# Kernel optimization log

Hardware: AMD Instinct MI355X
Metric: run time of the kernel (lower is better)

Reference implementation:

```python
import jax, jax.numpy as jnp
import numpy as np

M, N, EMB, H, ENC, T = 4096, 256, 64, 128, 128, 100


def _lstm_dir(x, Wih, Whh, b, h0, c0):
    # x: (T, M, E); PyTorch LSTM gate order i, f, g, o
    def step(carry, xt):
        h, c = carry
        g = xt @ Wih + h @ Whh + b
        i, f, gg, o = jnp.split(g, 4, axis=-1)
        c = jax.nn.sigmoid(f) * c + jax.nn.sigmoid(i) * jnp.tanh(gg)
        h = jax.nn.sigmoid(o) * jnp.tanh(c)
        return (h, c), h
    _, hs = jax.lax.scan(step, (h0, c0), x)
    return hs  # (T, M, H)


def setup_inputs() -> dict:
    key = jax.random.key(0)
    ks = jax.random.split(key, 14)
    rn = lambda k, sh, s: jax.random.normal(k, sh, jnp.float32) * s
    return {
        "lane_features": jax.random.normal(ks[0], (M, 600), jnp.float32),
        "obs_encoding": jax.random.normal(ks[1], (N, 128), jnp.float32),
        "embed_W": rn(ks[2], (4, EMB), 0.5),
        "embed_b": jnp.zeros((EMB,), jnp.float32),
        "attn_W": rn(ks[3], (128, 100), 0.09),
        "attn_b": jnp.zeros((100,), jnp.float32),
        "Wih_f": rn(ks[4], (EMB, 4 * H), 0.08),
        "Whh_f": rn(ks[5], (H, 4 * H), 0.08),
        "b_f": jnp.zeros((4 * H,), jnp.float32),
        "Wih_b": rn(ks[6], (EMB, 4 * H), 0.08),
        "Whh_b": rn(ks[7], (H, 4 * H), 0.08),
        "b_b": jnp.zeros((4 * H,), jnp.float32),
        "h0": rn(ks[8], (2, 1, H), 0.1),
        "c0": rn(ks[9], (2, 1, H), 0.1),
        "enc_W": rn(ks[10], (8 * H, ENC), 0.03),
        "enc_b": jnp.zeros((ENC,), jnp.float32),
        "same_obs_mask": jax.random.randint(ks[11], (M, 1), 0, N, jnp.int32),
    }


def reference(lane_features, obs_encoding, embed_W, embed_b, attn_W, attn_b,
              Wih_f, Whh_f, b_f, Wih_b, Whh_b, b_b, h0, c0, enc_W, enc_b,
              same_obs_mask):
    Mloc = lane_features.shape[0]
    E = embed_W.shape[1]
    Hh = Whh_f.shape[0]
    # last 400 features -> 100 timesteps x 4 features, then embed + relu
    feat = lane_features[:, -400:].reshape(Mloc * 100, 4)
    lane_embed = jax.nn.relu(feat @ embed_W + embed_b).reshape(Mloc, 100, E)
    # per-obstacle attention over the 100 lane points
    scores = jax.nn.softmax(jax.nn.relu(obs_encoding @ attn_W + attn_b), axis=1)  # (N, 100)
    # the original per-obs_id scatter loop == a single gather by obstacle id
    att = scores[same_obs_mask[:, 0]]  # (M, 100)
    x = jnp.transpose(lane_embed, (1, 0, 2))  # (T, M, E)
    h0f = jnp.broadcast_to(h0[0], (Mloc, Hh)); c0f = jnp.broadcast_to(c0[0], (Mloc, Hh))
    h0b = jnp.broadcast_to(h0[1], (Mloc, Hh)); c0b = jnp.broadcast_to(c0[1], (Mloc, Hh))
    hs_f = _lstm_dir(x, Wih_f, Whh_f, b_f, h0f, c0f)
    hs_b = _lstm_dir(x[::-1], Wih_b, Whh_b, b_b, h0b, c0b)[::-1]
    ls = jnp.transpose(jnp.concatenate([hs_f, hs_b], axis=-1), (1, 0, 2))  # (M, T, 2H)
    front = ls[:, 0, :]
    back = ls[:, -1, :]
    mx = jnp.max(ls, axis=1)
    attn_states = jnp.sum(ls * att[:, :, None], axis=1)
    out = jnp.concatenate([front, back, mx, attn_states], axis=1)  # (M, 8H)
    return jax.nn.relu(out @ enc_W + enc_b)
```

## Files before the change

kernel.cpp:

```cpp
#include <hip/hip_runtime.h>
#include <hip/hip_bf16.h>

#define MROWS 4096
#define TSTEPS 100
#define EMB 64
#define HID 128
#define GATES 512
#define KTOT 192
#define ROWS_PB 32
#define SROW 200
#define PSTR 520

typedef _Float16 half8 __attribute__((ext_vector_type(8)));
typedef _Float16 half4v __attribute__((ext_vector_type(4)));
typedef float f32x4 __attribute__((ext_vector_type(4)));

#define LOG2E  1.44269504f
#define LOG2E2 2.88539008f

__device__ __forceinline__ float rcpf(float x) { return __builtin_amdgcn_rcpf(x); }
__device__ __forceinline__ float ex2(float x) { return __builtin_amdgcn_exp2f(x); }

__global__ void prep_kernel(const float* __restrict__ obs,
                            const float* __restrict__ attn_W,
                            const float* __restrict__ attn_b,
                            float* __restrict__ scores,
                            const float* __restrict__ enc_W,
                            _Float16* __restrict__ frag) {
    const int tid = threadIdx.x;
    if (blockIdx.x < 256) {
        const int row = blockIdx.x;
        __shared__ float obs_s[128];
        __shared__ float red[128];

        if (tid < 128) obs_s[tid] = obs[row * 128 + tid];
        __syncthreads();

        float s = -1e30f;
        if (tid < 100) {
            float a = attn_b[tid];
            #pragma unroll 4
            for (int k = 0; k < 128; k++) a += obs_s[k] * attn_W[k * 100 + tid];
            s = fmaxf(a, 0.f);
        }
        if (tid < 128) red[tid] = s;
        __syncthreads();
        for (int off = 64; off > 0; off >>= 1) {
            if (tid < off) red[tid] = fmaxf(red[tid], red[tid + off]);
            __syncthreads();
        }
        const float m = red[0];
        __syncthreads();
        const float e = (tid < 100) ? __expf(s - m) : 0.f;
        if (tid < 128) red[tid] = e;
        __syncthreads();
        for (int off = 64; off > 0; off >>= 1) {
            if (tid < off) red[tid] += red[tid + off];
            __syncthreads();
        }
        const float inv = __fdividef(1.f, red[0]);
        if (tid < 100) scores[row * 100 + tid] = e * inv;
    } else {
        const int pb = blockIdx.x - 256;
        const int pair = pb * 16 + (tid >> 4);
        const int tile = pair >> 5;
        const int it   = pair & 31;
        const int sub  = tid & 15;
        #pragma unroll
        for (int li = 0; li < 4; li++) {
            const int l = sub * 4 + li;
            const int c = tile * 16 + (l & 15);
            const int kbase = it * 32 + (l >> 4) * 8;
            half8 v;
            #pragma unroll
            for (int j = 0; j < 8; j++) v[j] = (_Float16)enc_W[(kbase + j) * 128 + c];
            *(half8*)(frag + (((long)(tile * 32 + it)) * 64 + l) * 8) = v;
        }
    }
}

__launch_bounds__(512, 2)
__global__ void lstm_kernel(const float* __restrict__ lane_features,
                            const float* __restrict__ embed_W,
                            const float* __restrict__ embed_b,
                            const float* __restrict__ Wih_f,
                            const float* __restrict__ Whh_f,
                            const float* __restrict__ b_f,
                            const float* __restrict__ Wih_b,
                            const float* __restrict__ Whh_b,
                            const float* __restrict__ b_b,
                            const float* __restrict__ h0,
                            const float* __restrict__ c0,
                            const int*   __restrict__ mask,
                            const float* __restrict__ scores,
                            const _Float16* __restrict__ frag,
                            float* __restrict__ pacc) {
    const int blk = blockIdx.x;
    const int d = blk >> 7;
    const int rowbase = (blk & 127) * ROWS_PB;
    const int tid = threadIdx.x;
    const int wave = tid >> 6;
    const int lane = tid & 63;
    const int lane16 = lane & 15;
    const int quad = lane >> 4;

    const float* Wih = d ? Wih_b : Wih_f;
    const float* Whh = d ? Whh_b : Whh_f;
    const float* bia = d ? b_b : b_f;

    __shared__ __attribute__((aligned(16))) char smem[38400];
    auto panel = (_Float16 (*)[ROWS_PB][SROW])smem;
    float (*att_s)[32] = (float (*)[32])(smem + 25600);
    _Float16* pool = (_Float16*)smem;

    const int erow = tid >> 4;
    const int cc = (tid & 15) * 4;
    float ew_r[4][4], eb_r[4];
    #pragma unroll
    for (int j = 0; j < 4; j++) {
        #pragma unroll
        for (int jj = 0; jj < 4; jj++) ew_r[j][jj] = embed_W[j * EMB + cc + jj];
    }
    #pragma unroll
    for (int jj = 0; jj < 4; jj++) eb_r[jj] = embed_b[cc + jj];

    {
        const int r = tid >> 4, tcol = tid & 15;
        const int mr = mask[rowbase + r];
        for (int t = tcol; t < 100; t += 16) att_s[t][r] = scores[mr * 100 + t];
    }

    const int unitg = wave * 16 + lane16;
    half8 Bf[24];
    #pragma unroll
    for (int ct = 0; ct < 4; ct++) {
        const float scale = (ct == 2) ? LOG2E2 : LOG2E;
        const int col = ct * 128 + unitg;
        #pragma unroll
        for (int ki = 0; ki < 6; ki++) {
            half8 b;
            #pragma unroll
            for (int j = 0; j < 8; j++) {
                const int kk = ki * 32 + quad * 8 + j;
                const float w = (kk < EMB) ? Wih[kk * GATES + col]
                                           : Whh[(kk - EMB) * GATES + col];
                b[j] = (_Float16)(w * scale);
            }
            Bf[ct * 6 + ki] = b;
        }
    }
    f32x4 biasacc[4];
    #pragma unroll
    for (int ct = 0; ct < 4; ct++) {
        const float bg = bia[ct * 128 + unitg] * ((ct == 2) ? LOG2E2 : LOG2E);
        biasacc[ct] = (f32x4){bg, bg, bg, bg};
    }

    float cst[8], mx[8], as[8], h0s[8], hl[8];
    const float cinit = c0[d * 128 + unitg];
    #pragma unroll
    for (int p = 0; p < 8; p++) {
        cst[p] = cinit; mx[p] = -1e30f; as[p] = 0.f; h0s[p] = 0.f; hl[p] = 0.f;
    }

    for (int idx = tid; idx < ROWS_PB * HID; idx += 512) {
        const int r = idx >> 7, u = idx & 127;
        panel[0][r][EMB + u] = (_Float16)h0[d * 128 + u];
    }

    {
        const int t0 = d ? (TSTEPS - 1) : 0;
        const float4 fv = *(const float4*)(lane_features + (long)(rowbase + erow) * 600 + 200 + 4 * t0);
        half4v hv;
        #pragma unroll
        for (int jj = 0; jj < 4; jj++) {
            float e = eb_r[jj] + fv.x * ew_r[0][jj] + fv.y * ew_r[1][jj]
                               + fv.z * ew_r[2][jj] + fv.w * ew_r[3][jj];
            hv[jj] = (_Float16)fmaxf(e, 0.f);
        }
        *(half4v*)&panel[0][erow][cc] = hv;
    }
    __syncthreads();

    const float* fptr = lane_features + (long)(rowbase + erow) * 600 + 200
                      + (d ? 4 * (TSTEPS - 2) : 4);
    const int fstep = d ? -4 : 4;

#define HALF_STEP(PB, SE)                                                      \
    {                                                                          \
        const int se = (SE);                                                   \
        const int t = d ? (TSTEPS - 1 - se) : se;                              \
        float4 fv;                                                             \
        if (se < TSTEPS - 1) { fv = *(const float4*)fptr; fptr += fstep; }     \
        const f32x4 awv0 = *(const f32x4*)&att_s[t][quad * 4];                 \
        const f32x4 awv1 = *(const f32x4*)&att_s[t][16 + quad * 4];            \
        f32x4 acc[2][4];                                                       \
        _Pragma("unroll")                                                      \
        for (int ki = 0; ki < 6; ki++) {                                       \
            const half8 a0 = *(const half8*)&panel[PB][lane16][ki * 32 + quad * 8];      \
            const half8 a1 = *(const half8*)&panel[PB][16 + lane16][ki * 32 + quad * 8]; \
            _Pragma("unroll")                                                  \
            for (int ct = 0; ct < 4; ct++) {                                   \
                if (ki == 0) {                                                 \
                    acc[0][ct] = __builtin_amdgcn_mfma_f32_16x16x32_f16(a0, Bf[ct * 6], biasacc[ct], 0, 0, 0); \
                    acc[1][ct] = __builtin_amdgcn_mfma_f32_16x16x32_f16(a1, Bf[ct * 6], biasacc[ct], 0, 0, 0); \
                } else {                                                       \
                    acc[0][ct] = __builtin_amdgcn_mfma_f32_16x16x32_f16(a0, Bf[ct * 6 + ki], acc[0][ct], 0, 0, 0); \
                    acc[1][ct] = __builtin_amdgcn_mfma_f32_16x16x32_f16(a1, Bf[ct * 6 + ki], acc[1][ct], 0, 0, 0); \
                }                                                              \
            }                                                                  \
        }                                                                      \
        _Pragma("unroll")                                                      \
        for (int rt = 0; rt < 2; rt++) {                                       \
            _Pragma("unroll")                                                  \
            for (int r = 0; r < 4; r++) {                                      \
                const int pp = rt * 4 + r;                                     \
                const int row_local = rt * 16 + quad * 4 + r;                  \
                const float gi = acc[rt][0][r];                                \
                const float gf = acc[rt][1][r];                                \
                const float gg = fminf(acc[rt][2][r], 80.f);                   \
                const float go = acc[rt][3][r];                                \
                const float Ei = ex2(-gi);                                     \
                const float Ef = ex2(-gf);                                     \
                const float Eg = ex2(gg);                                      \
                const float Eo = ex2(-go);                                     \
                const float sf = rcpf(1.f + Ef);                               \
                const float r1 = rcpf((1.f + Ei) * (Eg + 1.f));                \
                const float cn = sf * cst[pp] + (Eg - 1.f) * r1;               \
                const float Ec = ex2(fminf(cn * LOG2E2, 80.f));                \
                const float r2 = rcpf((1.f + Eo) * (Ec + 1.f));                \
                const float h = (Ec - 1.f) * r2;                               \
                cst[pp] = cn;                                                  \
                hl[pp] = h;                                                    \
                mx[pp] = fmaxf(mx[pp], h);                                     \
                as[pp] = fmaf((rt ? awv1 : awv0)[r], h, as[pp]);               \
                panel[1 - (PB)][row_local][EMB + unitg] = (_Float16)h;         \
            }                                                                  \
        }                                                                      \
        if (se == 0) {                                                         \
            _Pragma("unroll")                                                  \
            for (int pp = 0; pp < 8; pp++) h0s[pp] = hl[pp];                   \
        }                                                                      \
        if (se < TSTEPS - 1) {                                                 \
            half4v hv;                                                         \
            _Pragma("unroll")                                                  \
            for (int jj = 0; jj < 4; jj++) {                                   \
                float e = eb_r[jj] + fv.x * ew_r[0][jj] + fv.y * ew_r[1][jj]   \
                                   + fv.z * ew_r[2][jj] + fv.w * ew_r[3][jj];  \
                hv[jj] = (_Float16)fmaxf(e, 0.f);                              \
            }                                                                  \
            *(half4v*)&panel[1 - (PB)][erow][cc] = hv;                         \
        }                                                                      \
        __syncthreads();                                                       \
    }

    for (int s = 0; s < TSTEPS; s += 2) {
        HALF_STEP(0, s)
        HALF_STEP(1, s + 1)
    }
#undef HALF_STEP

    #pragma unroll
    for (int pp = 0; pp < 8; pp++) {
        const int row_local = (pp >> 2) * 16 + quad * 4 + (pp & 3);
        const float fr = d ? hl[pp] : h0s[pp];
        const float bk = d ? h0s[pp] : hl[pp];
        pool[row_local * PSTR + 0 * 128 + unitg] = (_Float16)fr;
        pool[row_local * PSTR + 1 * 128 + unitg] = (_Float16)bk;
        pool[row_local * PSTR + 2 * 128 + unitg] = (_Float16)mx[pp];
        pool[row_local * PSTR + 3 * 128 + unitg] = (_Float16)as[pp];
    }
    __syncthreads();

    f32x4 cacc0 = {0.f, 0.f, 0.f, 0.f}, cacc1 = {0.f, 0.f, 0.f, 0.f};
    const _Float16* fbase = frag + ((long)wave * 32) * 64 * 8 + lane * 8;
    #pragma unroll
    for (int lc = 0; lc < 16; lc++) {
        const int seg = lc >> 2, c = lc & 3;
        const int itg = seg * 8 + d * 4 + c;
        const half8 b  = *(const half8*)(fbase + (long)itg * 64 * 8);
        const half8 a0 = *(const half8*)&pool[lane16 * PSTR + lc * 32 + quad * 8];
        const half8 a1 = *(const half8*)&pool[(16 + lane16) * PSTR + lc * 32 + quad * 8];
        cacc0 = __builtin_amdgcn_mfma_f32_16x16x32_f16(a0, b, cacc0, 0, 0, 0);
        cacc1 = __builtin_amdgcn_mfma_f32_16x16x32_f16(a1, b, cacc1, 0, 0, 0);
    }
    float* pacc_d = pacc + (long)d * MROWS * 128;
    #pragma unroll
    for (int r = 0; r < 4; r++) {
        pacc_d[(long)(rowbase + quad * 4 + r) * 128 + wave * 16 + lane16]      = cacc0[r];
        pacc_d[(long)(rowbase + 16 + quad * 4 + r) * 128 + wave * 16 + lane16] = cacc1[r];
    }
}

__global__ void final_kernel(const float* __restrict__ pacc,
                             const float* __restrict__ enc_b,
                             float* __restrict__ out) {
    const int idx = (blockIdx.x * 256 + threadIdx.x) * 4;
    const float4 a = *(const float4*)(pacc + idx);
    const float4 b = *(const float4*)(pacc + (long)MROWS * 128 + idx);
    const float4 bb = *(const float4*)(enc_b + (idx & 127));
    float4 o;
    o.x = fmaxf(a.x + b.x + bb.x, 0.f);
    o.y = fmaxf(a.y + b.y + bb.y, 0.f);
    o.z = fmaxf(a.z + b.z + bb.z, 0.f);
    o.w = fmaxf(a.w + b.w + bb.w, 0.f);
    *(float4*)(out + idx) = o;
}

extern "C" void kernel_launch(void* const* d_in, const int* in_sizes, int n_in,
                              void* d_out, int out_size, void* d_ws, size_t ws_size,
                              hipStream_t stream) {
    const float* lane_features = (const float*)d_in[0];
    const float* obs_encoding  = (const float*)d_in[1];
    const float* embed_W = (const float*)d_in[2];
    const float* embed_b = (const float*)d_in[3];
    const float* attn_W  = (const float*)d_in[4];
    const float* attn_b  = (const float*)d_in[5];
    const float* Wih_f   = (const float*)d_in[6];
    const float* Whh_f   = (const float*)d_in[7];
    const float* b_f     = (const float*)d_in[8];
    const float* Wih_b   = (const float*)d_in[9];
    const float* Whh_b   = (const float*)d_in[10];
    const float* b_b     = (const float*)d_in[11];
    const float* h0      = (const float*)d_in[12];
    const float* c0      = (const float*)d_in[13];
    const float* enc_W   = (const float*)d_in[14];
    const float* enc_b   = (const float*)d_in[15];
    const int*   mask    = (const int*)d_in[16];

    float*     scores = (float*)d_ws;
    _Float16*  frag   = (_Float16*)((char*)d_ws + (128 << 10));
    float*     pacc   = (float*)((char*)d_ws + (512 << 10));
    float*     out    = (float*)d_out;

    prep_kernel<<<272, 256, 0, stream>>>(obs_encoding, attn_W, attn_b, scores,
                                         enc_W, frag);
    lstm_kernel<<<256, 512, 0, stream>>>(lane_features, embed_W, embed_b,
                                         Wih_f, Whh_f, b_f, Wih_b, Whh_b, b_b,
                                         h0, c0, mask, scores, frag, pacc);
    final_kernel<<<512, 256, 0, stream>>>(pacc, enc_b, out);
}
```

Before: 286.9 us.

## Fuse attention softmax and final epilogue into LSTM kernel with atomic accumulation

Removes the separate attention-score pass by having each LSTM block compute the softmax attention for its own rows directly from obs_encoding. It also drops the final kernel: the two direction blocks atomically add their partial encoder outputs into a zeroed buffer, and the second block to arrive, detected through a per-tile counter, applies bias and ReLU. The prep kernel now only builds the fp16 fragments, staging them through shared memory, and zeroes pacc and the flags. In exchange, the attention work is recomputed redundantly per row in both directions, and the last-arriver pattern has no memory fence, so it may read stale pacc values.

```diff
diff --git a/kernel.cpp b/kernel.cpp
--- a/kernel.cpp
+++ b/kernel.cpp
@@ -21,61 +21,44 @@
 __device__ __forceinline__ float rcpf(float x) { return __builtin_amdgcn_rcpf(x); }
 __device__ __forceinline__ float ex2(float x) { return __builtin_amdgcn_exp2f(x); }
 
-__global__ void prep_kernel(const float* __restrict__ obs,
-                            const float* __restrict__ attn_W,
-                            const float* __restrict__ attn_b,
-                            float* __restrict__ scores,
-                            const float* __restrict__ enc_W,
-                            _Float16* __restrict__ frag) {
+__global__ void frag_prep_kernel(const float* __restrict__ enc_W,
+                                 _Float16* __restrict__ frag,
+                                 float* __restrict__ pacc,
+                                 int* __restrict__ flags) {
     const int tid = threadIdx.x;
-    if (blockIdx.x < 256) {
-        const int row = blockIdx.x;
-        __shared__ float obs_s[128];
-        __shared__ float red[128];
-
-        if (tid < 128) obs_s[tid] = obs[row * 128 + tid];
-        __syncthreads();
-
-        float s = -1e30f;
-        if (tid < 100) {
-            float a = attn_b[tid];
-            #pragma unroll 4
-            for (int k = 0; k < 128; k++) a += obs_s[k] * attn_W[k * 100 + tid];
-            s = fmaxf(a, 0.f);
-        }
-        if (tid < 128) red[tid] = s;
-        __syncthreads();
-        for (int off = 64; off > 0; off >>= 1) {
-            if (tid < off) red[tid] = fmaxf(red[tid], red[tid + off]);
-            __syncthreads();
-        }
-        const float m = red[0];
-        __syncthreads();
-        const float e = (tid < 100) ? __expf(s - m) : 0.f;
-        if (tid < 128) red[tid] = e;
-        __syncthreads();
-        for (int off = 64; off > 0; off >>= 1) {
-            if (tid < off) red[tid] += red[tid + off];
-            __syncthreads();
-        }
-        const float inv = __fdividef(1.f, red[0]);
-        if (tid < 100) scores[row * 100 + tid] = e * inv;
-    } else {
-        const int pb = blockIdx.x - 256;
-        const int pair = pb * 16 + (tid >> 4);
-        const int tile = pair >> 5;
-        const int it   = pair & 31;
-        const int sub  = tid & 15;
-        #pragma unroll
-        for (int li = 0; li < 4; li++) {
-            const int l = sub * 4 + li;
-            const int c = tile * 16 + (l & 15);
-            const int kbase = it * 32 + (l >> 4) * 8;
-            half8 v;
-            #pragma unroll
-            for (int j = 0; j < 8; j++) v[j] = (_Float16)enc_W[(kbase + j) * 128 + c];
-            *(half8*)(frag + (((long)(tile * 32 + it)) * 64 + l) * 8) = v;
-        }
+    if (blockIdx.x >= 16) {
+        const int z = blockIdx.x - 16;
+        const float4 zero = {0.f, 0.f, 0.f, 0.f};
+        #pragma unroll
+        for (int i = 0; i < 8; i++) {
+            *(float4*)(pacc + (long)z * 8192 + (i * 256 + tid) * 4) = zero;
+        }
+        if (blockIdx.x == 16 && tid < 128) flags[tid] = 0;
+        return;
+    }
+    const int pb = blockIdx.x;
+    __shared__ float tile[64][132];
+    #pragma unroll
+    for (int i = 0; i < 32; i++) {
+        const int idx = i * 256 + tid;
+        const int rr = idx >> 7, ccol = idx & 127;
+        tile[rr][ccol] = enc_W[(pb * 64 + rr) * 128 + ccol];
+    }
+    __syncthreads();
+    const int pair = tid >> 4;
+    const int tl = pair >> 1;
+    const int itl = pair & 1;
+    const int it = pb * 2 + itl;
+    const int sub = tid & 15;
+    #pragma unroll
+    for (int li = 0; li < 4; li++) {
+        const int l = sub * 4 + li;
+        const int c = tl * 16 + (l & 15);
+        const int kb = itl * 32 + (l >> 4) * 8;
+        half8 v;
+        #pragma unroll
+        for (int j = 0; j < 8; j++) v[j] = (_Float16)tile[kb + j][c];
+        *(half8*)(frag + (((long)(tl * 32 + it)) * 64 + l) * 8) = v;
     }
 }
 
@@ -92,9 +75,14 @@
                             const float* __restrict__ h0,
                             const float* __restrict__ c0,
                             const int*   __restrict__ mask,
-                            const float* __restrict__ scores,
+                            const float* __restrict__ obs,
+                            const float* __restrict__ attn_W,
+                            const float* __restrict__ attn_b,
+                            const float* __restrict__ enc_b,
                             const _Float16* __restrict__ frag,
-                            float* __restrict__ pacc) {
+                            float* __restrict__ pacc,
+                            int* __restrict__ flags,
+                            float* __restrict__ out) {
     const int blk = blockIdx.x;
     const int d = blk >> 7;
     const int rowbase = (blk & 127) * ROWS_PB;
@@ -111,6 +99,7 @@
     __shared__ __attribute__((aligned(16))) char smem[38400];
     auto panel = (_Float16 (*)[ROWS_PB][SROW])smem;
     float (*att_s)[32] = (float (*)[32])(smem + 25600);
+    float (*red)[16] = (float (*)[16])(smem + 12800);
     _Float16* pool = (_Float16*)smem;
 
     const int erow = tid >> 4;
@@ -125,9 +114,55 @@
     for (int jj = 0; jj < 4; jj++) eb_r[jj] = embed_b[cc + jj];
 
     {
-        const int r = tid >> 4, tcol = tid & 15;
+        const int r = tid >> 4;
+        const int tcol = tid & 15;
         const int mr = mask[rowbase + r];
-        for (int t = tcol; t < 100; t += 16) att_s[t][r] = scores[mr * 100 + t];
+        const float* obsrow = obs + mr * 128;
+        float a[7];
+        #pragma unroll
+        for (int j = 0; j < 7; j++) {
+            const int t = tcol + j * 16;
+            a[j] = (t < 100) ? attn_b[t] : 0.f;
+        }
+        #pragma unroll 4
+        for (int k = 0; k < 128; k++) {
+            const float ov = obsrow[k];
+            #pragma unroll
+            for (int j = 0; j < 7; j++) {
+                const int t = tcol + j * 16;
+                a[j] = fmaf(ov, attn_W[k * 100 + (t < 100 ? t : 99)], a[j]);
+            }
+        }
+        float s_loc[7];
+        float lm = -1e30f;
+        #pragma unroll
+        for (int j = 0; j < 7; j++) {
+            const int t = tcol + j * 16;
+            s_loc[j] = (t < 100) ? fmaxf(a[j], 0.f) : -1e30f;
+            lm = fmaxf(lm, s_loc[j]);
+        }
+        red[r][tcol] = lm;
+        __syncthreads();
+        float m = -1e30f;
+        #pragma unroll
+        for (int j = 0; j < 16; j++) m = fmaxf(m, red[r][j]);
+        __syncthreads();
+        float ls = 0.f;
+        #pragma unroll
+        for (int j = 0; j < 7; j++) {
+            if (tcol + j * 16 < 100) ls += ex2((s_loc[j] - m) * LOG2E);
+        }
+        red[r][tcol] = ls;
+        __syncthreads();
+        float Z = 0.f;
+        #pragma unroll
+        for (int j = 0; j < 16; j++) Z += red[r][j];
+        const float rz = rcpf(Z);
+        #pragma unroll
+        for (int j = 0; j < 7; j++) {
+            const int t = tcol + j * 16;
+            if (t < 100) att_s[t][r] = ex2((s_loc[j] - m) * LOG2E) * rz;
+        }
     }
 
     const int unitg = wave * 16 + lane16;
@@ -284,27 +319,27 @@
         cacc0 = __builtin_amdgcn_mfma_f32_16x16x32_f16(a0, b, cacc0, 0, 0, 0);
         cacc1 = __builtin_amdgcn_mfma_f32_16x16x32_f16(a1, b, cacc1, 0, 0, 0);
     }
-    float* pacc_d = pacc + (long)d * MROWS * 128;
+
+    const int col = wave * 16 + lane16;
     #pragma unroll
     for (int r = 0; r < 4; r++) {
-        pacc_d[(long)(rowbase + quad * 4 + r) * 128 + wave * 16 + lane16]      = cacc0[r];
-        pacc_d[(long)(rowbase + 16 + quad * 4 + r) * 128 + wave * 16 + lane16] = cacc1[r];
-    }
-}
-
-__global__ void final_kernel(const float* __restrict__ pacc,
-                             const float* __restrict__ enc_b,
-                             float* __restrict__ out) {
-    const int idx = (blockIdx.x * 256 + threadIdx.x) * 4;
-    const float4 a = *(const float4*)(pacc + idx);
-    const float4 b = *(const float4*)(pacc + (long)MROWS * 128 + idx);
-    const float4 bb = *(const float4*)(enc_b + (idx & 127));
-    float4 o;
-    o.x = fmaxf(a.x + b.x + bb.x, 0.f);
-    o.y = fmaxf(a.y + b.y + bb.y, 0.f);
-    o.z = fmaxf(a.z + b.z + bb.z, 0.f);
-    o.w = fmaxf(a.w + b.w + bb.w, 0.f);
-    *(float4*)(out + idx) = o;
+        atomicAdd(&pacc[(long)(rowbase + quad * 4 + r) * 128 + col], cacc0[r]);
+        atomicAdd(&pacc[(long)(rowbase + 16 + quad * 4 + r) * 128 + col], cacc1[r]);
+    }
+    __syncthreads();
+    int* lf = (int*)smem;
+    if (tid == 0) lf[0] = atomicAdd(&flags[blk & 127], 1);
+    __syncthreads();
+    if (lf[0] == 1) {
+        const float bb = enc_b[col];
+        #pragma unroll
+        for (int r = 0; r < 4; r++) {
+            const long i0 = (long)(rowbase + quad * 4 + r) * 128 + col;
+            const long i1 = (long)(rowbase + 16 + quad * 4 + r) * 128 + col;
+            out[i0] = fmaxf(pacc[i0] + bb, 0.f);
+            out[i1] = fmaxf(pacc[i1] + bb, 0.f);
+        }
+    }
 }
 
 extern "C" void kernel_launch(void* const* d_in, const int* in_sizes, int n_in,
@@ -328,15 +363,14 @@
     const float* enc_b   = (const float*)d_in[15];
     const int*   mask    = (const int*)d_in[16];
 
-    float*     scores = (float*)d_ws;
-    _Float16*  frag   = (_Float16*)((char*)d_ws + (128 << 10));
-    float*     pacc   = (float*)((char*)d_ws + (512 << 10));
-    float*     out    = (float*)d_out;
-
-    prep_kernel<<<272, 256, 0, stream>>>(obs_encoding, attn_W, attn_b, scores,
-                                         enc_W, frag);
+    _Float16*  frag  = (_Float16*)d_ws;
+    int*       flags = (int*)((char*)d_ws + (256 << 10));
+    float*     pacc  = (float*)((char*)d_ws + (512 << 10));
+    float*     out   = (float*)d_out;
+
+    frag_prep_kernel<<<80, 256, 0, stream>>>(enc_W, frag, pacc, flags);
     lstm_kernel<<<256, 512, 0, stream>>>(lane_features, embed_W, embed_b,
                                          Wih_f, Whh_f, b_f, Wih_b, Whh_b, b_b,
-                                         h0, c0, mask, scores, frag, pacc);
-    final_kernel<<<512, 256, 0, stream>>>(pacc, enc_b, out);
+                                         h0, c0, mask, obs_encoding, attn_W,
+                                         attn_b, enc_b, frag, pacc, flags, out);
 }
```

After: 291.8 us. No clear change (+1.7%).

## Fuse final reduction into LSTM kernel via atomics and last-block flag

Applied to the files above, without the earlier changes.

Removes the separate final kernel. Each direction block now atomically adds its partial encoder output into a zeroed accumulator, and whichever of the two blocks for a row tile arrives second (found through a counter flag) applies bias and ReLU and writes the output. The prep kernel gains extra blocks that zero the accumulator and flags, and its enc_W transpose now goes through shared memory for coalesced loads. The LSTM cell step is also reordered so the first row tile's MFMAs finish before the second's, letting gate math overlap with the remaining matrix work. The costs are global atomics and a last-arriver pattern whose correctness depends on memory ordering between the atomic adds and the flag increment.

```diff
diff --git a/kernel.cpp b/kernel.cpp
--- a/kernel.cpp
+++ b/kernel.cpp
@@ -26,7 +26,9 @@
                             const float* __restrict__ attn_b,
                             float* __restrict__ scores,
                             const float* __restrict__ enc_W,
-                            _Float16* __restrict__ frag) {
+                            _Float16* __restrict__ frag,
+                            float* __restrict__ pacc,
+                            int* __restrict__ flags) {
     const int tid = threadIdx.x;
     if (blockIdx.x < 256) {
         const int row = blockIdx.x;
@@ -60,22 +62,39 @@
         }
         const float inv = __fdividef(1.f, red[0]);
         if (tid < 100) scores[row * 100 + tid] = e * inv;
-    } else {
+    } else if (blockIdx.x < 272) {
         const int pb = blockIdx.x - 256;
-        const int pair = pb * 16 + (tid >> 4);
-        const int tile = pair >> 5;
-        const int it   = pair & 31;
-        const int sub  = tid & 15;
+        __shared__ float tile[64][132];
+        #pragma unroll
+        for (int i = 0; i < 32; i++) {
+            const int idx = i * 256 + tid;
+            const int rr = idx >> 7, ccol = idx & 127;
+            tile[rr][ccol] = enc_W[(pb * 64 + rr) * 128 + ccol];
+        }
+        __syncthreads();
+        const int pair = tid >> 4;
+        const int tl = pair >> 1;
+        const int itl = pair & 1;
+        const int it = pb * 2 + itl;
+        const int sub = tid & 15;
         #pragma unroll
         for (int li = 0; li < 4; li++) {
             const int l = sub * 4 + li;
-            const int c = tile * 16 + (l & 15);
-            const int kbase = it * 32 + (l >> 4) * 8;
+            const int c = tl * 16 + (l & 15);
+            const int kb = itl * 32 + (l >> 4) * 8;
             half8 v;
             #pragma unroll
-            for (int j = 0; j < 8; j++) v[j] = (_Float16)enc_W[(kbase + j) * 128 + c];
-            *(half8*)(frag + (((long)(tile * 32 + it)) * 64 + l) * 8) = v;
-        }
+            for (int j = 0; j < 8; j++) v[j] = (_Float16)tile[kb + j][c];
+            *(half8*)(frag + (((long)(tl * 32 + it)) * 64 + l) * 8) = v;
+        }
+    } else {
+        const int z = blockIdx.x - 272;
+        const float4 zero = {0.f, 0.f, 0.f, 0.f};
+        #pragma unroll
+        for (int i = 0; i < 8; i++) {
+            *(float4*)(pacc + (long)z * 8192 + (i * 256 + tid) * 4) = zero;
+        }
+        if (blockIdx.x == 272 && tid < 128) flags[tid] = 0;
     }
 }
 
@@ -93,8 +112,11 @@
                             const float* __restrict__ c0,
                             const int*   __restrict__ mask,
                             const float* __restrict__ scores,
+                            const float* __restrict__ enc_b,
                             const _Float16* __restrict__ frag,
-                            float* __restrict__ pacc) {
+                            float* __restrict__ pacc,
+                            int* __restrict__ flags,
+                            float* __restrict__ out) {
     const int blk = blockIdx.x;
     const int d = blk >> 7;
     const int rowbase = (blk & 127) * ROWS_PB;
@@ -186,57 +208,60 @@
                       + (d ? 4 * (TSTEPS - 2) : 4);
     const int fstep = d ? -4 : 4;
 
+#define CELL_RT(RT, ACC, AWV)                                                  \
+    _Pragma("unroll")                                                          \
+    for (int r = 0; r < 4; r++) {                                              \
+        const int pp = (RT) * 4 + r;                                           \
+        const int row_local = (RT) * 16 + quad * 4 + r;                        \
+        const float gi = ACC[0][r];                                            \
+        const float gf = ACC[1][r];                                            \
+        const float gg = fminf(ACC[2][r], 80.f);                               \
+        const float go = ACC[3][r];                                            \
+        const float Ei = ex2(-gi);                                             \
+        const float Ef = ex2(-gf);                                             \
+        const float Eg = ex2(gg);                                              \
+        const float Eo = ex2(-go);                                             \
+        const float sf = rcpf(1.f + Ef);                                       \
+        const float r1 = rcpf((1.f + Ei) * (Eg + 1.f));                        \
+        const float cn = sf * cst[pp] + (Eg - 1.f) * r1;                       \
+        const float Ec = ex2(fminf(cn * LOG2E2, 80.f));                        \
+        const float r2 = rcpf((1.f + Eo) * (Ec + 1.f));                        \
+        const float h = (Ec - 1.f) * r2;                                       \
+        cst[pp] = cn;                                                          \
+        hl[pp] = h;                                                            \
+        mx[pp] = fmaxf(mx[pp], h);                                             \
+        as[pp] = fmaf((AWV)[r], h, as[pp]);                                    \
+        panel[1 - (PB_)][row_local][EMB + unitg] = (_Float16)h;                \
+    }
+
 #define HALF_STEP(PB, SE)                                                      \
     {                                                                          \
+        const int PB_ = (PB);                                                  \
         const int se = (SE);                                                   \
         const int t = d ? (TSTEPS - 1 - se) : se;                              \
         float4 fv;                                                             \
         if (se < TSTEPS - 1) { fv = *(const float4*)fptr; fptr += fstep; }     \
         const f32x4 awv0 = *(const f32x4*)&att_s[t][quad * 4];                 \
         const f32x4 awv1 = *(const f32x4*)&att_s[t][16 + quad * 4];            \
-        f32x4 acc[2][4];                                                       \
+        f32x4 acc0[4], acc1[4];                                                \
         _Pragma("unroll")                                                      \
         for (int ki = 0; ki < 6; ki++) {                                       \
             const half8 a0 = *(const half8*)&panel[PB][lane16][ki * 32 + quad * 8];      \
+            _Pragma("unroll")                                                  \
+            for (int ct = 0; ct < 4; ct++)                                     \
+                acc0[ct] = __builtin_amdgcn_mfma_f32_16x16x32_f16(             \
+                    a0, Bf[ct * 6 + ki], (ki == 0) ? biasacc[ct] : acc0[ct], 0, 0, 0); \
+        }                                                                      \
+        _Pragma("unroll")                                                      \
+        for (int ki = 0; ki < 6; ki++) {                                       \
             const half8 a1 = *(const half8*)&panel[PB][16 + lane16][ki * 32 + quad * 8]; \
             _Pragma("unroll")                                                  \
-            for (int ct = 0; ct < 4; ct++) {                                   \
-                if (ki == 0) {                                                 \
-                    acc[0][ct] = __builtin_amdgcn_mfma_f32_16x16x32_f16(a0, Bf[ct * 6], biasacc[ct], 0, 0, 0); \
-                    acc[1][ct] = __builtin_amdgcn_mfma_f32_16x16x32_f16(a1, Bf[ct * 6], biasacc[ct], 0, 0, 0); \
-                } else {                                                       \
-                    acc[0][ct] = __builtin_amdgcn_mfma_f32_16x16x32_f16(a0, Bf[ct * 6 + ki], acc[0][ct], 0, 0, 0); \
-                    acc[1][ct] = __builtin_amdgcn_mfma_f32_16x16x32_f16(a1, Bf[ct * 6 + ki], acc[1][ct], 0, 0, 0); \
-                }                                                              \
-            }                                                                  \
+            for (int ct = 0; ct < 4; ct++)                                     \
+                acc1[ct] = __builtin_amdgcn_mfma_f32_16x16x32_f16(             \
+                    a1, Bf[ct * 6 + ki], (ki == 0) ? biasacc[ct] : acc1[ct], 0, 0, 0); \
         }                                                                      \
-        _Pragma("unroll")                                                      \
-        for (int rt = 0; rt < 2; rt++) {                                       \
-            _Pragma("unroll")                                                  \
-            for (int r = 0; r < 4; r++) {                                      \
-                const int pp = rt * 4 + r;                                     \
-                const int row_local = rt * 16 + quad * 4 + r;                  \
-                const float gi = acc[rt][0][r];                                \
-                const float gf = acc[rt][1][r];                                \
-                const float gg = fminf(acc[rt][2][r], 80.f);                   \
-                const float go = acc[rt][3][r];                                \
-                const float Ei = ex2(-gi);                                     \
-                const float Ef = ex2(-gf);                                     \
-                const float Eg = ex2(gg);                                      \
-                const float Eo = ex2(-go);                                     \
-                const float sf = rcpf(1.f + Ef);                               \
-                const float r1 = rcpf((1.f + Ei) * (Eg + 1.f));                \
-                const float cn = sf * cst[pp] + (Eg - 1.f) * r1;               \
-                const float Ec = ex2(fminf(cn * LOG2E2, 80.f));                \
-                const float r2 = rcpf((1.f + Eo) * (Ec + 1.f));                \
-                const float h = (Ec - 1.f) * r2;                               \
-                cst[pp] = cn;                                                  \
-                hl[pp] = h;                                                    \
-                mx[pp] = fmaxf(mx[pp], h);                                     \
-                as[pp] = fmaf((rt ? awv1 : awv0)[r], h, as[pp]);               \
-                panel[1 - (PB)][row_local][EMB + unitg] = (_Float16)h;         \
-            }                                                                  \
-        }                                                                      \
+        CELL_RT(0, acc0, awv0)                                                 \
+        CELL_RT(1, acc1, awv1)                                                 \
         if (se == 0) {                                                         \
             _Pragma("unroll")                                                  \
             for (int pp = 0; pp < 8; pp++) h0s[pp] = hl[pp];                   \
@@ -259,6 +284,7 @@
         HALF_STEP(1, s + 1)
     }
 #undef HALF_STEP
+#undef CELL_RT
 
     #pragma unroll
     for (int pp = 0; pp < 8; pp++) {
@@ -284,27 +310,27 @@
         cacc0 = __builtin_amdgcn_mfma_f32_16x16x32_f16(a0, b, cacc0, 0, 0, 0);
         cacc1 = __builtin_amdgcn_mfma_f32_16x16x32_f16(a1, b, cacc1, 0, 0, 0);
     }
-    float* pacc_d = pacc + (long)d * MROWS * 128;
+
+    const int col = wave * 16 + lane16;
     #pragma unroll
     for (int r = 0; r < 4; r++) {
-        pacc_d[(long)(rowbase + quad * 4 + r) * 128 + wave * 16 + lane16]      = cacc0[r];
-        pacc_d[(long)(rowbase + 16 + quad * 4 + r) * 128 + wave * 16 + lane16] = cacc1[r];
-    }
-}
-
-__global__ void final_kernel(const float* __restrict__ pacc,
-                             const float* __restrict__ enc_b,
-                             float* __restrict__ out) {
-    const int idx = (blockIdx.x * 256 + threadIdx.x) * 4;
-    const float4 a = *(const float4*)(pacc + idx);
-    const float4 b = *(const float4*)(pacc + (long)MROWS * 128 + idx);
-    const float4 bb = *(const float4*)(enc_b + (idx & 127));
-    float4 o;
-    o.x = fmaxf(a.x + b.x + bb.x, 0.f);
-    o.y = fmaxf(a.y + b.y + bb.y, 0.f);
-    o.z = fmaxf(a.z + b.z + bb.z, 0.f);
-    o.w = fmaxf(a.w + b.w + bb.w, 0.f);
-    *(float4*)(out + idx) = o;
+        atomicAdd(&pacc[(long)(rowbase + quad * 4 + r) * 128 + col], cacc0[r]);
+        atomicAdd(&pacc[(long)(rowbase + 16 + quad * 4 + r) * 128 + col], cacc1[r]);
+    }
+    __syncthreads();
+    int* lf = (int*)smem;
+    if (tid == 0) lf[0] = atomicAdd(&flags[blk & 127], 1);
+    __syncthreads();
+    if (lf[0] == 1) {
+        const float bb = enc_b[col];
+        #pragma unroll
+        for (int r = 0; r < 4; r++) {
+            const long i0 = (long)(rowbase + quad * 4 + r) * 128 + col;
+            const long i1 = (long)(rowbase + 16 + quad * 4 + r) * 128 + col;
+            out[i0] = fmaxf(pacc[i0] + bb, 0.f);
+            out[i1] = fmaxf(pacc[i1] + bb, 0.f);
+        }
+    }
 }
 
 extern "C" void kernel_launch(void* const* d_in, const int* in_sizes, int n_in,
@@ -330,13 +356,14 @@
 
     float*     scores = (float*)d_ws;
     _Float16*  frag   = (_Float16*)((char*)d_ws + (128 << 10));
+    int*       flags  = (int*)((char*)d_ws + (448 << 10));
     float*     pacc   = (float*)((char*)d_ws + (512 << 10));
     float*     out    = (float*)d_out;
 
-    prep_kernel<<<272, 256, 0, stream>>>(obs_encoding, attn_W, attn_b, scores,
-                                         enc_W, frag);
+    prep_kernel<<<336, 256, 0, stream>>>(obs_encoding, attn_W, attn_b, scores,
+                                         enc_W, frag, pacc, flags);
     lstm_kernel<<<256, 512, 0, stream>>>(lane_features, embed_W, embed_b,
                                          Wih_f, Whh_f, b_f, Wih_b, Whh_b, b_b,
-                                         h0, c0, mask, scores, frag, pacc);
-    final_kernel<<<512, 256, 0, stream>>>(pacc, enc_b, out);
+                                         h0, c0, mask, scores, enc_b,
+                                         frag, pacc, flags, out);
 }
```

After: 295.9 us. 3.1% more time.
